# Kernel optimization log

Hardware: AMD Instinct MI355X
Metric: run time of the kernel (lower is better)

## Reference

```python
import jax, jax.numpy as jnp
import numpy as np

B, S, E, A = 32, 1000, 1024, 512


def setup_inputs() -> dict:
    key = jax.random.key(0)
    ks = jax.random.split(key, 7)
    sc = 0.02
    return {
        "x": jax.random.normal(ks[0], (B, S, E), dtype=jnp.float32),
        "Wk": jax.random.normal(ks[1], (E, A), dtype=jnp.float32) * sc,
        "bk": jax.random.normal(ks[2], (A,), dtype=jnp.float32) * sc,
        "Wq": jax.random.normal(ks[3], (E, A), dtype=jnp.float32) * sc,
        "bq": jax.random.normal(ks[4], (A,), dtype=jnp.float32) * sc,
        "Wv": jax.random.normal(ks[5], (E, A), dtype=jnp.float32) * sc,
        "bv": jax.random.normal(ks[6], (A,), dtype=jnp.float32) * sc,
    }


def reference(x, Wk, bk, Wq, bq, Wv, bv):
    seq = x.shape[1]
    k = x @ Wk + bk          # [B,S,A]
    q = x @ Wq + bq          # [B,S,A]
    v = x @ Wv + bv          # [B,S,A]
    # NOTE: module scales by sqrt(sequence), not sqrt(attention_dim)
    den = jnp.asarray(seq, x.dtype) ** 0.5
    scores = jnp.einsum("bqa,bka->bqk", q, k) / den  # [B,S,S]
    causal = jnp.tril(jnp.ones((seq, seq), dtype=bool))
    scores = jnp.where(causal, scores, -jnp.inf)
    attn = jax.nn.softmax(scores, axis=-1)
    return jnp.einsum("bqk,bka->bqa", attn, v)      # [B,S,A]
```

## Files before the change

### kernel.cpp

```cpp
#include <hip/hip_runtime.h>
#include <hip/hip_bf16.h>
#include <stdint.h>

#define DEVI __device__ __forceinline__

typedef short s16x8 __attribute__((ext_vector_type(8)));
typedef short s16x4 __attribute__((ext_vector_type(4)));
typedef float f32x4 __attribute__((ext_vector_type(4)));

static constexpr int BB = 32, SS = 1000, EE = 1024, AA = 512;
static constexpr int MM = BB * SS;

static constexpr size_t OFF_X16 = 0;
static constexpr size_t OFF_Q   = OFF_X16 + (size_t)MM * EE * 2;
static constexpr size_t OFF_K   = OFF_Q  + (size_t)MM * AA * 2;
static constexpr size_t OFF_VT  = OFF_K  + (size_t)MM * AA * 2;
static constexpr size_t OFF_WT  = OFF_VT + (size_t)BB * AA * SS * 2;

static constexpr int PROWS = BB * 3 * 128;
static constexpr size_t ML_OFF = (size_t)2 * PROWS * 512;

DEVI unsigned short f2bf(float f) {
  union { float f; unsigned int u; } c; c.f = f;
  unsigned int u = c.u + 0x7fffu + ((c.u >> 16) & 1u);
  return (unsigned short)(u >> 16);
}

DEVI void gl_lds16(const void* g, void* l) {
  __builtin_amdgcn_global_load_lds(
      (const __attribute__((address_space(1))) unsigned int*)g,
      (__attribute__((address_space(3))) unsigned int*)l, 16, 0, 0);
}

DEVI void wg_barrier() {
  asm volatile("" ::: "memory");
  __builtin_amdgcn_s_barrier();
  asm volatile("" ::: "memory");
}

DEVI float fast_exp2(float x) {
#if __has_builtin(__builtin_amdgcn_exp2f)
  return __builtin_amdgcn_exp2f(x);
#else
  return __builtin_exp2f(x);
#endif
}

__global__ __launch_bounds__(256) void x_to_bf16_kernel(const float* __restrict__ x,
                                                        unsigned short* __restrict__ x16) {
  const long n4 = (long)MM * EE / 4;
  long i = (long)blockIdx.x * blockDim.x + threadIdx.x;
  const long stride = (long)gridDim.x * blockDim.x;
  for (; i < n4; i += stride) {
    const float4 v = ((const float4*)x)[i];
    ushort4 o;
    o.x = f2bf(v.x); o.y = f2bf(v.y); o.z = f2bf(v.z); o.w = f2bf(v.w);
    ((ushort4*)x16)[i] = o;
  }
}

__global__ __launch_bounds__(256) void wt_kernel(const float* __restrict__ Wq,
                                                 const float* __restrict__ Wk,
                                                 const float* __restrict__ Wv,
                                                 unsigned short* __restrict__ WT) {
  const float* W = (blockIdx.z == 0) ? Wq : (blockIdx.z == 1) ? Wk : Wv;
  unsigned short* out = WT + (size_t)blockIdx.z * AA * EE;
  __shared__ unsigned short t[64][65];
  const int k0 = blockIdx.x * 64, n0 = blockIdx.y * 64;
  #pragma unroll
  for (int i = 0; i < 16; ++i) {
    int idx = i * 256 + threadIdx.x;
    int r = idx >> 6, c = idx & 63;
    t[r][c] = f2bf(W[(size_t)(k0 + r) * AA + n0 + c]);
  }
  __syncthreads();
  #pragma unroll
  for (int i = 0; i < 16; ++i) {
    int idx = i * 256 + threadIdx.x;
    int r = idx >> 6, c = idx & 63;
    out[(size_t)(n0 + r) * EE + k0 + c] = t[c][r];
  }
}

__global__ __launch_bounds__(256, 2) void proj_kernel(
    const unsigned short* __restrict__ X16, const unsigned short* __restrict__ WT,
    const float* __restrict__ bq, const float* __restrict__ bk, const float* __restrict__ bv,
    unsigned short* __restrict__ Qo, unsigned short* __restrict__ Ko,
    unsigned short* __restrict__ VTo) {
  constexpr int BK = 64, NKT = EE / BK;
  __shared__ unsigned char lds[65536];
  unsigned char* ldsA = lds;
  unsigned char* ldsB = lds + 32768;
  const int tid = threadIdx.x, lane = tid & 63, wave = tid >> 6;
  const int id = blockIdx.x;
  const int r12 = id % 12;
  const int z = r12 >> 2;
  const int m0 = (id / 12) * 128, n0 = (r12 & 3) * 128;
  const unsigned short* Wz = WT + (size_t)z * AA * EE;

  f32x4 acc[4][4];
  #pragma unroll
  for (int i = 0; i < 4; ++i)
    #pragma unroll
    for (int j = 0; j < 4; ++j) acc[i][j] = f32x4{0.f, 0.f, 0.f, 0.f};

  auto stage = [&](int buf, int kt) {
    #pragma unroll
    for (int i = 0; i < 4; ++i) {
      int c = i * 256 + tid;
      int row = c >> 3;
      int cb = ((c & 7) * 16) ^ ((row & 7) << 4);
      gl_lds16(X16 + (size_t)(m0 + row) * EE + kt * BK + (cb >> 1), ldsA + buf * 16384 + c * 16);
    }
    #pragma unroll
    for (int i = 0; i < 4; ++i) {
      int c = i * 256 + tid;
      int row = c >> 3;
      int cb = ((c & 7) * 16) ^ ((row & 7) << 4);
      gl_lds16(Wz + (size_t)(n0 + row) * EE + kt * BK + (cb >> 1), ldsB + buf * 16384 + c * 16);
    }
  };

  auto compute = [&](int buf) {
    #pragma unroll
    for (int kk = 0; kk < 2; ++kk) {
      s16x8 a[4], b[4];
      #pragma unroll
      for (int m = 0; m < 4; ++m) {
        int row = (wave >> 1) * 64 + m * 16 + (lane & 15);
        int cb = (kk * 64 + (lane >> 4) * 16) ^ ((row & 7) << 4);
        a[m] = *(const s16x8*)(ldsA + buf * 16384 + row * 128 + cb);
      }
      #pragma unroll
      for (int n = 0; n < 4; ++n) {
        int row = (wave & 1) * 64 + n * 16 + (lane & 15);
        int cb = (kk * 64 + (lane >> 4) * 16) ^ ((row & 7) << 4);
        b[n] = *(const s16x8*)(ldsB + buf * 16384 + row * 128 + cb);
      }
      #pragma unroll
      for (int m = 0; m < 4; ++m)
        #pragma unroll
        for (int n = 0; n < 4; ++n)
          acc[m][n] = __builtin_amdgcn_mfma_f32_16x16x32_bf16(a[m], b[n], acc[m][n], 0, 0, 0);
    }
  };

  stage(0, 0);
  for (int kt = 0; kt < NKT; ++kt) {
    const int cur = kt & 1;
    if (kt + 1 < NKT) {
      stage(cur ^ 1, kt + 1);
      asm volatile("s_waitcnt vmcnt(8)" ::: "memory");
    } else {
      asm volatile("s_waitcnt vmcnt(0)" ::: "memory");
    }
    wg_barrier();
    compute(cur);
    wg_barrier();
  }

  const float* bias = (z == 0) ? bq : (z == 1) ? bk : bv;
  const float scale = (z == 0) ? 0.04562280215f : 1.0f;
  unsigned short* T = (unsigned short*)lds;
  const int rbase = (wave >> 1) * 64 + (lane >> 4) * 4;
  const int cbase = (wave & 1) * 64 + (lane & 15);
  float bvals[4];
  #pragma unroll
  for (int n = 0; n < 4; ++n) bvals[n] = bias[n0 + cbase + n * 16];
  #pragma unroll
  for (int m = 0; m < 4; ++m) {
    #pragma unroll
    for (int n = 0; n < 4; ++n) {
      const int cl = cbase + n * 16;
      #pragma unroll
      for (int j = 0; j < 4; ++j) {
        const int rl = rbase + m * 16 + j;
        const unsigned short h = f2bf((acc[m][n][j] + bvals[n]) * scale);
        if (z == 2) T[cl * 136 + rl] = h;
        else        T[rl * 136 + cl] = h;
      }
    }
  }
  wg_barrier();
  #pragma unroll
  for (int i = 0; i < 8; ++i) {
    int c2 = i * 256 + tid;
    int r = c2 >> 4, ch = (c2 & 15) * 8;
    s16x8 chunk = *(const s16x8*)&T[r * 136 + ch];
    if (z == 2) {
      const int rowg0 = m0 + ch;
      const int bb2 = rowg0 / SS, ss2 = rowg0 - bb2 * SS;
      *(s16x8*)&VTo[(size_t)bb2 * AA * SS + (size_t)(n0 + r) * SS + ss2] = chunk;
    } else {
      unsigned short* O = (z == 0) ? Qo : Ko;
      *(s16x8*)&O[(size_t)(m0 + r) * AA + n0 + ch] = chunk;
    }
  }
}

__global__ __launch_bounds__(512, 2) void attn_kernel(
    const unsigned short* __restrict__ Qs, const unsigned short* __restrict__ Ks,
    const unsigned short* __restrict__ VT, float* __restrict__ out,
    float* __restrict__ part) {
  constexpr int KVB = 32;
  __shared__ unsigned char ldsK[2][KVB * AA * 2];
  __shared__ unsigned char ldsV[2][AA * KVB * 2];
  __shared__ unsigned char ldsP[8][16 * 80];

  const int tid = threadIdx.x, lane = tid & 63, wave = tid >> 6;
  const int L = blockIdx.x;
  const int b = L & 31;
  const int g = 7 - (L >> 5);

  const unsigned short* kbase = Ks + (size_t)b * SS * AA;
  const unsigned short* vbase = VT + (size_t)b * AA * SS;
  unsigned int koff[4], voff[4];
  #pragma unroll
  for (int i = 0; i < 4; ++i) {
    int c = i * 512 + tid;
    int r = c >> 6;
    int cb = ((c & 63) * 16) ^ ((r & 7) << 4);
    koff[i] = r * AA + (cb >> 1);
    int pair = c >> 3;
    int within = (c & 7) * 16;
    int half = within >> 6;
    int kb = (within & 63) ^ ((pair & 3) << 4);
    int a_ = pair * 2 + half;
    voff[i] = a_ * SS + (kb >> 1);
  }

  auto stageKV = [&](int buf, int t) {
    #pragma unroll
    for (int i = 0; i < 4; ++i)
      gl_lds16(kbase + koff[i] + (unsigned)(t * (KVB * AA)),
               &ldsK[buf][(i * 512 + tid) * 16]);
    #pragma unroll
    for (int i = 0; i < 4; ++i)
      gl_lds16(vbase + voff[i] + (unsigned)(t * KVB),
               &ldsV[buf][(i * 512 + tid) * 16]);
  };

  int ownN = 4 * (g + 1);
  int rb_[2], t0_[2], t1_[2], md_[2], cx_[2];
  int nph = 1;
  rb_[0] = 128 * g; t0_[0] = 0; t1_[0] = (ownN < 20) ? ownN : 20;
  md_[0] = (g <= 4) ? 0 : 1; cx_[0] = g - 5;
  if (g <= 2) {
    int r = 7 - g;
    rb_[1] = 128 * r; t0_[1] = 20; t1_[1] = 4 * (r + 1); md_[1] = 2; cx_[1] = r - 5;
    nph = 2;
  }

  for (int ph = 0; ph < nph; ++ph) {
    const int rowbase = rb_[ph], tbeg = t0_[ph], tend = t1_[ph];
    const int mode = md_[ph], cidx = cx_[ph];
    const int q0w = rowbase + wave * 16;

    s16x8 qf[16];
    {
      int qrow = q0w + (lane & 15);
      int qr = qrow < SS ? qrow : SS - 1;
      const unsigned short* qp = Qs + (size_t)(b * SS + qr) * AA + (lane >> 4) * 8;
      #pragma unroll
      for (int f = 0; f < 16; ++f) qf[f] = *(const s16x8*)(qp + f * 32);
    }

    f32x4 o[32];
    #pragma unroll
    for (int n = 0; n < 32; ++n) o[n] = f32x4{0.f, 0.f, 0.f, 0.f};
    float mrun[4], ps[4];
    #pragma unroll
    for (int j = 0; j < 4; ++j) { mrun[j] = -__builtin_inff(); ps[j] = 0.f; }

    stageKV(0, tbeg);
    asm volatile("s_waitcnt vmcnt(0)" ::: "memory");
    wg_barrier();

    for (int t = tbeg; t < tend; ++t) {
      const int cur = (t - tbeg) & 1;
      const int k0 = t * KVB;
      if (t + 1 < tend) stageKV(cur ^ 1, t + 1);

      f32x4 p0a = {0.f, 0.f, 0.f, 0.f}, p0b = {0.f, 0.f, 0.f, 0.f};
      f32x4 p1a = {0.f, 0.f, 0.f, 0.f}, p1b = {0.f, 0.f, 0.f, 0.f};
      {
        const int r0 = lane & 15;
        const int sw = (r0 & 7) << 4;
        const int kb16 = (lane >> 4) * 16;
        const int rb0 = r0 << 10, rb1 = (r0 + 16) << 10;
        #pragma unroll
        for (int f = 0; f < 8; ++f) {
          const int offA = f * 64 + kb16;
          const int offB = (f + 8) * 64 + kb16;
          s16x8 k0A = *(const s16x8*)&ldsK[cur][rb0 + (offA ^ sw)];
          s16x8 k1A = *(const s16x8*)&ldsK[cur][rb1 + (offA ^ sw)];
          s16x8 k0B = *(const s16x8*)&ldsK[cur][rb0 + (offB ^ sw)];
          s16x8 k1B = *(const s16x8*)&ldsK[cur][rb1 + (offB ^ sw)];
          p0a = __builtin_amdgcn_mfma_f32_16x16x32_bf16(qf[f], k0A, p0a, 0, 0, 0);
          p1a = __builtin_amdgcn_mfma_f32_16x16x32_bf16(qf[f], k1A, p1a, 0, 0, 0);
          p0b = __builtin_amdgcn_mfma_f32_16x16x32_bf16(qf[f + 8], k0B, p0b, 0, 0, 0);
          p1b = __builtin_amdgcn_mfma_f32_16x16x32_bf16(qf[f + 8], k1B, p1b, 0, 0, 0);
        }
      }
      f32x4 p0 = p0a + p0b, p1 = p1a + p1b;

      const int kcol = k0 + (lane & 15);
      float lm[4];
      #pragma unroll
      for (int j = 0; j < 4; ++j) {
        const int q = q0w + (lane >> 4) * 4 + j;
        float s0 = p0[j], s1 = p1[j];
        if (kcol > q || kcol >= SS) s0 = -__builtin_inff();
        if (kcol + 16 > q || kcol + 16 >= SS) s1 = -__builtin_inff();
        p0[j] = s0; p1[j] = s1;
        lm[j] = fmaxf(s0, s1);
      }
      const int myneed = (lm[0] > mrun[0] + 8.f) | (lm[1] > mrun[1] + 8.f) |
                         (lm[2] > mrun[2] + 8.f) | (lm[3] > mrun[3] + 8.f);
      if (__any(myneed)) {
        float rm[4] = {lm[0], lm[1], lm[2], lm[3]};
        #pragma unroll
        for (int st = 1; st <= 8; st <<= 1)
          #pragma unroll
          for (int j = 0; j < 4; ++j) rm[j] = fmaxf(rm[j], __shfl_xor(rm[j], st));
        float corr[4];
        #pragma unroll
        for (int j = 0; j < 4; ++j) {
          const float mnew = fmaxf(mrun[j], rm[j]);
          corr[j] = fast_exp2(mrun[j] - mnew);
          mrun[j] = mnew;
          ps[j] *= corr[j];
        }
        #pragma unroll
        for (int n = 0; n < 32; ++n)
          #pragma unroll
          for (int j = 0; j < 4; ++j) o[n][j] *= corr[j];
      }
      #pragma unroll
      for (int j = 0; j < 4; ++j) {
        const float e0 = fast_exp2(p0[j] - mrun[j]);
        const float e1 = fast_exp2(p1[j] - mrun[j]);
        ps[j] += e0 + e1;
        p0[j] = e0; p1[j] = e1;
      }

      {
        unsigned short* pb = (unsigned short*)&ldsP[wave][0];
        const int prow = (lane >> 4) * 4, pc = lane & 15;
        #pragma unroll
        for (int j = 0; j < 4; ++j) {
          pb[(prow + j) * 40 + pc]      = f2bf(p0[j]);
          pb[(prow + j) * 40 + pc + 16] = f2bf(p1[j]);
        }
      }
      s16x8 pa;
      {
        const unsigned char* pp = &ldsP[wave][(lane & 15) * 80 + (lane >> 4) * 16];
        s16x4 lo = *(const s16x4*)pp;
        s16x4 hi = *(const s16x4*)(pp + 8);
        pa = s16x8{lo[0], lo[1], lo[2], lo[3], hi[0], hi[1], hi[2], hi[3]};
      }

      #pragma unroll
      for (int n = 0; n < 32; ++n) {
        const int a_ = n * 16 + (lane & 15);
        const int pair = a_ >> 1;
        const int off = pair * 128 + (a_ & 1) * 64 + (((lane >> 4) * 16) ^ ((pair & 3) << 4));
        s16x8 vb = *(const s16x8*)&ldsV[cur][off];
        o[n] = __builtin_amdgcn_mfma_f32_16x16x32_bf16(pa, vb, o[n], 0, 0, 0);
      }

      asm volatile("s_waitcnt vmcnt(0)" ::: "memory");
      wg_barrier();
    }

    #pragma unroll
    for (int st = 1; st <= 8; st <<= 1)
      #pragma unroll
      for (int j = 0; j < 4; ++j) ps[j] += __shfl_xor(ps[j], st);

    if (mode == 0) {
      #pragma unroll
      for (int j = 0; j < 4; ++j) {
        const int q = q0w + (lane >> 4) * 4 + j;
        if (q < SS) {
          const float inv = 1.0f / ps[j];
          float* op = out + (size_t)(b * SS + q) * AA + (lane & 15);
          #pragma unroll
          for (int n = 0; n < 32; ++n) op[n * 16] = o[n][j] * inv;
        }
      }
    } else {
      const int slot = mode - 1;
      #pragma unroll
      for (int j = 0; j < 4; ++j) {
        const int rl = wave * 16 + (lane >> 4) * 4 + j;
        const size_t idx = (size_t)slot * PROWS + ((size_t)(b * 3 + cidx) * 128 + rl);
        float* po = part + idx * 512 + (lane & 15);
        #pragma unroll
        for (int n = 0; n < 32; ++n) po[n * 16] = o[n][j];
        if ((lane & 15) == 0) {
          float* pml = part + ML_OFF + idx * 2;
          pml[0] = mrun[j];
          pml[1] = ps[j];
        }
      }
    }
  }
}

__global__ __launch_bounds__(256) void combine_kernel(const float* __restrict__ part,
                                                      float* __restrict__ out) {
  const int rid = blockIdx.x * 2 + (threadIdx.x >> 7);
  const int t = threadIdx.x & 127;
  const int b = rid / 384;
  const int rem = rid - b * 384;
  const int c = rem >> 7, row = rem & 127;
  const int q = (c + 5) * 128 + row;
  if (q >= SS) return;
  const float* mlA = part + ML_OFF + (size_t)rid * 2;
  const float* mlB = part + ML_OFF + ((size_t)PROWS + rid) * 2;
  const float mA = mlA[0], lA = mlA[1];
  const float mB = mlB[0], lB = mlB[1];
  const float m = fmaxf(mA, mB);
  const float sA = fast_exp2(mA - m), sB = fast_exp2(mB - m);
  const float inv = 1.0f / (lA * sA + lB * sB);
  const float4 a = ((const float4*)(part + (size_t)rid * 512))[t];
  const float4 d = ((const float4*)(part + ((size_t)PROWS + rid) * 512))[t];
  float4 r;
  r.x = (a.x * sA + d.x * sB) * inv;
  r.y = (a.y * sA + d.y * sB) * inv;
  r.z = (a.z * sA + d.z * sB) * inv;
  r.w = (a.w * sA + d.w * sB) * inv;
  ((float4*)(out + ((size_t)b * SS + q) * AA))[t] = r;
}

extern "C" void kernel_launch(void* const* d_in, const int* in_sizes, int n_in,
                              void* d_out, int out_size, void* d_ws, size_t ws_size,
                              hipStream_t stream) {
  const float* x  = (const float*)d_in[0];
  const float* Wk = (const float*)d_in[1];
  const float* bk = (const float*)d_in[2];
  const float* Wq = (const float*)d_in[3];
  const float* bq = (const float*)d_in[4];
  const float* Wv = (const float*)d_in[5];
  const float* bv = (const float*)d_in[6];

  char* ws = (char*)d_ws;
  unsigned short* X16 = (unsigned short*)(ws + OFF_X16);
  unsigned short* Qw  = (unsigned short*)(ws + OFF_Q);
  unsigned short* Kw  = (unsigned short*)(ws + OFF_K);
  unsigned short* VTw = (unsigned short*)(ws + OFF_VT);
  unsigned short* WT  = (unsigned short*)(ws + OFF_WT);
  float* Part = (float*)(ws + OFF_X16);

  x_to_bf16_kernel<<<dim3(2048), dim3(256), 0, stream>>>(x, X16);
  wt_kernel<<<dim3(EE / 64, AA / 64, 3), dim3(256), 0, stream>>>(Wq, Wk, Wv, WT);
  proj_kernel<<<dim3(3000), dim3(256), 0, stream>>>(
      X16, WT, bq, bk, bv, Qw, Kw, VTw);
  attn_kernel<<<dim3(256), dim3(512), 0, stream>>>(Qw, Kw, VTw, (float*)d_out, Part);
  combine_kernel<<<dim3(PROWS / 2), dim3(256), 0, stream>>>(Part, (float*)d_out);
}
```

Measured before the change: 301.1 us.

## Restructure projection GEMM into 256x256 tiles with 8-phase interleaved pipeline

The QKV projection kernel moves from 128x128 tiles with 256 threads to 256x256 tiles with 512 threads, using a 128KB double-buffered LDS. The K loop becomes eight phases that each stage a half-tile while the MFMAs run, and it uses s_setprio around the compute. Blocks are remapped so that groups of 8 row tiles share the same weight columns, which improves L2 reuse. The larger tiles cut global and LDS traffic per FLOP, but they raise register pressure and allow only one block per CU because of LDS, and the epilogue now runs in two halves.

```diff
diff --git a/kernel.cpp b/kernel.cpp
--- a/kernel.cpp
+++ b/kernel.cpp
@@ -82,118 +82,162 @@
   }
 }
 
-__global__ __launch_bounds__(256, 2) void proj_kernel(
+#define PROJ_PHASE(BUF, QA, QB, SKT, SWH, SBUF, DOVM)                          \
+  {                                                                            \
+    if ((QB) == 0) {                                                           \
+      _Pragma("unroll") for (int kk = 0; kk < 2; ++kk) {                       \
+        _Pragma("unroll") for (int f = 0; f < 4; ++f) {                        \
+          int row = wm * 128 + ((QA) * 4 + f) * 16 + (lane & 15);              \
+          int cb = (kk * 64 + (lane >> 4) * 16) ^ ((row & 7) << 4);            \
+          aR[kk][f] = *(const s16x8*)(lds + (BUF) * 32768 + row * 128 + cb);   \
+        }                                                                      \
+      }                                                                        \
+    }                                                                          \
+    s16x8 bR[2][2];                                                            \
+    _Pragma("unroll") for (int kk = 0; kk < 2; ++kk) {                         \
+      _Pragma("unroll") for (int g2 = 0; g2 < 2; ++g2) {                       \
+        int row = wn * 64 + ((QB) * 2 + g2) * 16 + (lane & 15);                \
+        int cb = (kk * 64 + (lane >> 4) * 16) ^ ((row & 7) << 4);              \
+        bR[kk][g2] = *(const s16x8*)(lds + 65536 + (BUF) * 32768 + row * 128 + cb); \
+      }                                                                        \
+    }                                                                          \
+    if ((SKT) >= 0) stage_half(SBUF, SKT, SWH);                                \
+    wg_barrier();                                                              \
+    __builtin_amdgcn_s_setprio(1);                                             \
+    _Pragma("unroll") for (int kk = 0; kk < 2; ++kk) {                         \
+      _Pragma("unroll") for (int f = 0; f < 4; ++f) {                          \
+        _Pragma("unroll") for (int g2 = 0; g2 < 2; ++g2) {                     \
+          acc[(QA) * 4 + f][(QB) * 2 + g2] = __builtin_amdgcn_mfma_f32_16x16x32_bf16( \
+              aR[kk][f], bR[kk][g2], acc[(QA) * 4 + f][(QB) * 2 + g2], 0, 0, 0); \
+        }                                                                      \
+      }                                                                        \
+    }                                                                          \
+    __builtin_amdgcn_s_setprio(0);                                             \
+    if (DOVM) asm volatile("s_waitcnt vmcnt(0)" ::: "memory");                 \
+    wg_barrier();                                                              \
+  }
+
+__global__ __launch_bounds__(512, 2) void proj_kernel(
     const unsigned short* __restrict__ X16, const unsigned short* __restrict__ WT,
     const float* __restrict__ bq, const float* __restrict__ bk, const float* __restrict__ bv,
     unsigned short* __restrict__ Qo, unsigned short* __restrict__ Ko,
     unsigned short* __restrict__ VTo) {
-  constexpr int BK = 64, NKT = EE / BK;
-  __shared__ unsigned char lds[65536];
-  unsigned char* ldsA = lds;
-  unsigned char* ldsB = lds + 32768;
+  __shared__ unsigned char lds[131072];
   const int tid = threadIdx.x, lane = tid & 63, wave = tid >> 6;
-  const int id = blockIdx.x;
-  const int r12 = id % 12;
-  const int z = r12 >> 2;
-  const int m0 = (id / 12) * 128, n0 = (r12 & 3) * 128;
+  const int wm = wave >> 2, wn = wave & 3;
+
+  const int phys = blockIdx.x;
+  int p, r;
+  if (phys < 720) { int g = phys / 48, w = phys % 48; p = g * 8 + (w & 7); r = w >> 3; }
+  else            { int w = phys - 720; p = 120 + w % 5; r = w / 5; }
+  const int z = r >> 1, nidx = r & 1;
+  const int m0 = p * 256, n0 = nidx * 256;
   const unsigned short* Wz = WT + (size_t)z * AA * EE;
 
-  f32x4 acc[4][4];
+  f32x4 acc[8][4];
   #pragma unroll
-  for (int i = 0; i < 4; ++i)
+  for (int i = 0; i < 8; ++i)
     #pragma unroll
     for (int j = 0; j < 4; ++j) acc[i][j] = f32x4{0.f, 0.f, 0.f, 0.f};
 
-  auto stage = [&](int buf, int kt) {
-    #pragma unroll
-    for (int i = 0; i < 4; ++i) {
-      int c = i * 256 + tid;
-      int row = c >> 3;
-      int cb = ((c & 7) * 16) ^ ((row & 7) << 4);
-      gl_lds16(X16 + (size_t)(m0 + row) * EE + kt * BK + (cb >> 1), ldsA + buf * 16384 + c * 16);
-    }
-    #pragma unroll
-    for (int i = 0; i < 4; ++i) {
-      int c = i * 256 + tid;
-      int row = c >> 3;
-      int cb = ((c & 7) * 16) ^ ((row & 7) << 4);
-      gl_lds16(Wz + (size_t)(n0 + row) * EE + kt * BK + (cb >> 1), ldsB + buf * 16384 + c * 16);
-    }
+  unsigned int offH[2];
+  #pragma unroll
+  for (int i = 0; i < 2; ++i) {
+    int c = i * 512 + tid;
+    int rl = c >> 3, s = c & 7;
+    int cb = (s * 16) ^ ((rl & 7) << 4);
+    offH[i] = (unsigned)(rl * EE + (cb >> 1));
+  }
+  auto stage_half = [&](int buf, int kt, int which) {
+    const int h = which & 1;
+    const int isB = which >> 1;
+    const unsigned short* srcb = isB ? (Wz + (size_t)(n0 + h * 128) * EE + kt * 64)
+                                     : (X16 + (size_t)(m0 + h * 128) * EE + kt * 64);
+    unsigned char* dstb = lds + (isB ? 65536 : 0) + buf * 32768 + h * 16384;
+    #pragma unroll
+    for (int i = 0; i < 2; ++i)
+      gl_lds16(srcb + offH[i], dstb + (i * 512 + tid) * 16);
   };
 
-  auto compute = [&](int buf) {
-    #pragma unroll
-    for (int kk = 0; kk < 2; ++kk) {
-      s16x8 a[4], b[4];
-      #pragma unroll
-      for (int m = 0; m < 4; ++m) {
-        int row = (wave >> 1) * 64 + m * 16 + (lane & 15);
-        int cb = (kk * 64 + (lane >> 4) * 16) ^ ((row & 7) << 4);
-        a[m] = *(const s16x8*)(ldsA + buf * 16384 + row * 128 + cb);
-      }
-      #pragma unroll
-      for (int n = 0; n < 4; ++n) {
-        int row = (wave & 1) * 64 + n * 16 + (lane & 15);
-        int cb = (kk * 64 + (lane >> 4) * 16) ^ ((row & 7) << 4);
-        b[n] = *(const s16x8*)(ldsB + buf * 16384 + row * 128 + cb);
-      }
-      #pragma unroll
-      for (int m = 0; m < 4; ++m)
-        #pragma unroll
-        for (int n = 0; n < 4; ++n)
-          acc[m][n] = __builtin_amdgcn_mfma_f32_16x16x32_bf16(a[m], b[n], acc[m][n], 0, 0, 0);
-    }
-  };
-
-  stage(0, 0);
-  for (int kt = 0; kt < NKT; ++kt) {
-    const int cur = kt & 1;
-    if (kt + 1 < NKT) {
-      stage(cur ^ 1, kt + 1);
-      asm volatile("s_waitcnt vmcnt(8)" ::: "memory");
-    } else {
-      asm volatile("s_waitcnt vmcnt(0)" ::: "memory");
-    }
-    wg_barrier();
-    compute(cur);
-    wg_barrier();
+  stage_half(0, 0, 0); stage_half(0, 0, 1); stage_half(0, 0, 2); stage_half(0, 0, 3);
+  asm volatile("s_waitcnt vmcnt(0)" ::: "memory");
+  wg_barrier();
+
+  s16x8 aR[2][4];
+  for (int J = 0; J < 8; ++J) {
+    const int t1 = 2 * J + 1;
+    const int t2 = (J < 7) ? (2 * J + 2) : -1;
+    PROJ_PHASE(0, 0, 0, t1, 0, 1, false)
+    PROJ_PHASE(0, 0, 1, t1, 1, 1, false)
+    PROJ_PHASE(0, 1, 0, t1, 2, 1, false)
+    PROJ_PHASE(0, 1, 1, t1, 3, 1, true)
+    PROJ_PHASE(1, 0, 0, t2, 0, 0, false)
+    PROJ_PHASE(1, 0, 1, t2, 1, 0, false)
+    PROJ_PHASE(1, 1, 0, t2, 2, 0, false)
+    PROJ_PHASE(1, 1, 1, t2, 3, 0, true)
   }
 
   const float* bias = (z == 0) ? bq : (z == 1) ? bk : bv;
   const float scale = (z == 0) ? 0.04562280215f : 1.0f;
   unsigned short* T = (unsigned short*)lds;
-  const int rbase = (wave >> 1) * 64 + (lane >> 4) * 4;
-  const int cbase = (wave & 1) * 64 + (lane & 15);
-  float bvals[4];
+  float bv4[4];
   #pragma unroll
-  for (int n = 0; n < 4; ++n) bvals[n] = bias[n0 + cbase + n * 16];
-  #pragma unroll
-  for (int m = 0; m < 4; ++m) {
-    #pragma unroll
-    for (int n = 0; n < 4; ++n) {
-      const int cl = cbase + n * 16;
-      #pragma unroll
-      for (int j = 0; j < 4; ++j) {
-        const int rl = rbase + m * 16 + j;
-        const unsigned short h = f2bf((acc[m][n][j] + bvals[n]) * scale);
-        if (z == 2) T[cl * 136 + rl] = h;
-        else        T[rl * 136 + cl] = h;
-      }
+  for (int nf = 0; nf < 4; ++nf) bv4[nf] = bias[n0 + wn * 64 + nf * 16 + (lane & 15)];
+
+  if (z != 2) {
+    unsigned short* O = (z == 0) ? Qo : Ko;
+    #pragma unroll
+    for (int h = 0; h < 2; ++h) {
+      if (wm == h) {
+        #pragma unroll
+        for (int mf = 0; mf < 8; ++mf)
+          #pragma unroll
+          for (int nf = 0; nf < 4; ++nf) {
+            const int col = wn * 64 + nf * 16 + (lane & 15);
+            #pragma unroll
+            for (int j = 0; j < 4; ++j) {
+              const int rr = mf * 16 + (lane >> 4) * 4 + j;
+              T[rr * 264 + col] = f2bf((acc[mf][nf][j] + bv4[nf]) * scale);
+            }
+          }
+      }
+      wg_barrier();
+      #pragma unroll
+      for (int i = 0; i < 8; ++i) {
+        int c2 = i * 512 + tid;
+        int rr = c2 >> 5, ch = (c2 & 31) * 8;
+        s16x8 chunk = *(const s16x8*)&T[rr * 264 + ch];
+        *(s16x8*)&O[(size_t)(m0 + h * 128 + rr) * AA + n0 + ch] = chunk;
+      }
+      wg_barrier();
     }
-  }
-  wg_barrier();
-  #pragma unroll
-  for (int i = 0; i < 8; ++i) {
-    int c2 = i * 256 + tid;
-    int r = c2 >> 4, ch = (c2 & 15) * 8;
-    s16x8 chunk = *(const s16x8*)&T[r * 136 + ch];
-    if (z == 2) {
-      const int rowg0 = m0 + ch;
-      const int bb2 = rowg0 / SS, ss2 = rowg0 - bb2 * SS;
-      *(s16x8*)&VTo[(size_t)bb2 * AA * SS + (size_t)(n0 + r) * SS + ss2] = chunk;
-    } else {
-      unsigned short* O = (z == 0) ? Qo : Ko;
-      *(s16x8*)&O[(size_t)(m0 + r) * AA + n0 + ch] = chunk;
+  } else {
+    #pragma unroll
+    for (int h = 0; h < 2; ++h) {
+      if ((wn >> 1) == h) {
+        #pragma unroll
+        for (int mf = 0; mf < 8; ++mf)
+          #pragma unroll
+          for (int nf = 0; nf < 4; ++nf) {
+            const int al = (wn & 1) * 64 + nf * 16 + (lane & 15);
+            #pragma unroll
+            for (int j = 0; j < 4; ++j) {
+              const int sl = wm * 128 + mf * 16 + (lane >> 4) * 4 + j;
+              T[al * 264 + sl] = f2bf(acc[mf][nf][j] + bv4[nf]);
+            }
+          }
+      }
+      wg_barrier();
+      #pragma unroll
+      for (int i = 0; i < 8; ++i) {
+        int c2 = i * 512 + tid;
+        int rr = c2 >> 5, ch = (c2 & 31) * 8;
+        s16x8 chunk = *(const s16x8*)&T[rr * 264 + ch];
+        const int rowg0 = m0 + ch;
+        const int bb2 = rowg0 / SS, ss2 = rowg0 - bb2 * SS;
+        *(s16x8*)&VTo[(size_t)bb2 * AA * SS + (size_t)(n0 + h * 128 + rr) * SS + ss2] = chunk;
+      }
+      wg_barrier();
     }
   }
 }
@@ -456,7 +500,7 @@
 
   x_to_bf16_kernel<<<dim3(2048), dim3(256), 0, stream>>>(x, X16);
   wt_kernel<<<dim3(EE / 64, AA / 64, 3), dim3(256), 0, stream>>>(Wq, Wk, Wv, WT);
-  proj_kernel<<<dim3(3000), dim3(256), 0, stream>>>(
+  proj_kernel<<<dim3(750), dim3(512), 0, stream>>>(
       X16, WT, bq, bk, bv, Qw, Kw, VTw);
   attn_kernel<<<dim3(256), dim3(512), 0, stream>>>(Qw, Kw, VTw, (float*)d_out, Part);
   combine_kernel<<<dim3(PROWS / 2), dim3(256), 0, stream>>>(Part, (float*)d_out);
```

After: 276.5 us. -8.2%, faster.
